# Performance work log

Measured on AMD Instinct MI355X. Metric: run time of the kernel, lower is better.

The kernel has to match this reference:

```python
import jax, jax.numpy as jnp
import numpy as np

B, D, T, K = 16, 512, 4096, 1024

def setup_inputs() -> dict:
    key = jax.random.key(0)
    kx, kc = jax.random.split(key)
    x = jax.random.normal(kx, (B, D, T), dtype=jnp.float32)
    codebook = jax.random.normal(kc, (K, D), dtype=jnp.float32)
    return {"x": x, "codebook": codebook}

def reference(x, codebook):
    # x: [B, D, T] -> xt: [B, T, D]
    xt = jnp.transpose(x, (0, 2, 1))
    x_sq = jnp.sum(xt * xt, axis=-1, keepdims=True)          # [B, T, 1]
    c_sq = jnp.sum(codebook * codebook, axis=-1)             # [K]
    cross = jnp.einsum('btd,kd->btk', xt, codebook)          # [B, T, K]
    dist = x_sq - 2.0 * cross + c_sq                         # [B, T, K]
    indexes = jnp.argmin(dist, axis=2)                       # [B, T] int
    quantized = codebook[indexes]                            # [B, T, D]
    quantized = jnp.transpose(quantized, (0, 2, 1))          # [B, D, T]
    return quantized, indexes
```

## Files before the change

kernel.cpp:

```cpp
#include <hip/hip_runtime.h>

#define BB 16
#define DD 512
#define TT 4096
#define KK 1024

typedef _Float16 h16;
typedef __attribute__((ext_vector_type(8))) _Float16 half8;
typedef __attribute__((ext_vector_type(4))) float float4v;

#define XTH_OFF 0ull
#define XTL_OFF 67108864ull
#define CBH_OFF 134217728ull
#define CBL_OFF 135266304ull
#define CSQ_OFF 136314880ull
#define WS_NEED (136314880ull + 4096ull)

#define GLOAD_LDS16(g, l) __builtin_amdgcn_global_load_lds( \
    (const __attribute__((address_space(1))) void*)(g),      \
    (__attribute__((address_space(3))) void*)(l), 16, 0, 0)

__global__ void csq_kernel(const float* __restrict__ cb, float* __restrict__ csq) {
    int wave = threadIdx.x >> 6;
    int lane = threadIdx.x & 63;
    int row  = blockIdx.x * 4 + wave;
    const float* r = cb + (size_t)row * DD;
    float s = 0.f;
    #pragma unroll
    for (int i = 0; i < DD / 64; ++i) { float v = r[lane + i * 64]; s += v * v; }
    #pragma unroll
    for (int off = 32; off; off >>= 1) s += __shfl_down(s, off, 64);
    if (lane == 0) csq[row] = s;
}

__global__ __launch_bounds__(256) void split_x_kernel(const float* __restrict__ x,
                                                      h16* __restrict__ xth,
                                                      h16* __restrict__ xtl) {
    __shared__ float xs[32][132];
    const int tb = blockIdx.x, dcb = blockIdx.y, b = blockIdx.z;
    const int tid = threadIdx.x;
    const int t0 = tb * 128, d0 = dcb * 32;
    const float* xp = x + ((size_t)b * DD + d0) * TT + t0;
    #pragma unroll
    for (int j = 0; j < 4; ++j) {
        int i4 = tid + 256 * j;
        int dd = i4 >> 5, c4 = (i4 & 31) << 2;
        *(float4*)&xs[dd][c4] = *(const float4*)(xp + (size_t)dd * TT + c4);
    }
    __syncthreads();
    const int r = tid >> 1;
    const int ch = (tid & 1) * 16;
    h16 hv[16], lv[16];
    #pragma unroll
    for (int i = 0; i < 16; ++i) {
        float v = xs[ch + i][r];
        h16 h = (h16)v;
        hv[i] = h;
        lv[i] = (h16)(v - (float)h);
    }
    size_t o = (((size_t)(b * 32 + tb) * 16) + dcb) * 4096 + (size_t)tid * 16;
    *(half8*)(xth + o)     = *(half8*)&hv[0];
    *(half8*)(xth + o + 8) = *(half8*)&hv[8];
    *(half8*)(xtl + o)     = *(half8*)&lv[0];
    *(half8*)(xtl + o + 8) = *(half8*)&lv[8];
}

__global__ __launch_bounds__(256) void split_cb_kernel(const float* __restrict__ cb,
                                                       h16* __restrict__ cbh,
                                                       h16* __restrict__ cbl) {
    const int kb = blockIdx.x >> 4, dcb = blockIdx.x & 15;
    const int tid = threadIdx.x;
    const float* cp = cb + ((size_t)kb * 128) * DD + dcb * 32;
    h16* oh = cbh + ((size_t)(kb * 16 + dcb)) * 4096;
    h16* ol = cbl + ((size_t)(kb * 16 + dcb)) * 4096;
    #pragma unroll
    for (int j = 0; j < 4; ++j) {
        int i4 = tid + 256 * j;
        int rr = i4 >> 3, c4 = (i4 & 7) << 2;
        float4 v = *(const float4*)(cp + (size_t)rr * DD + c4);
        float vv[4] = {v.x, v.y, v.z, v.w};
        h16 h[4], l[4];
        #pragma unroll
        for (int i = 0; i < 4; ++i) {
            h[i] = (h16)vv[i];
            l[i] = (h16)(vv[i] - (float)h[i]);
        }
        *(ushort4*)(oh + rr * 32 + c4) = *(ushort4*)h;
        *(ushort4*)(ol + rr * 32 + c4) = *(ushort4*)l;
    }
}

__global__ __launch_bounds__(512, 4) void mfma_argmin_kernel(
    const h16* __restrict__ xth, const h16* __restrict__ xtl,
    const h16* __restrict__ cbh, const h16* __restrict__ cbl,
    const float* __restrict__ csq, const float* __restrict__ cb,
    float* __restrict__ idx_f_out, float* __restrict__ out) {

    __shared__ h16 ash[2][4096];
    __shared__ h16 asl[2][4096];
    __shared__ h16 bsh[2][4096];
    __shared__ h16 bsl[2][4096];
    __shared__ float redv[4][128];
    __shared__ int   redi[4][128];

    const int tid = threadIdx.x;
    const int wid = tid >> 6, lane = tid & 63;
    const int wm = wid & 1;
    const int wn = wid >> 1;
    const int tb = blockIdx.x, b = blockIdx.y;
    const int t0 = tb * 128;
    const int c  = lane & 15;
    const int q  = lane >> 4;

    const h16* aH = xth + ((size_t)(b * 32 + tb) * 16) * 4096;
    const h16* aL = xtl + ((size_t)(b * 32 + tb) * 16) * 4096;

    const int soff = tid * 8;

    GLOAD_LDS16(aH  + soff,        &ash[0][soff]);
    GLOAD_LDS16(aL  + soff,        &asl[0][soff]);
    GLOAD_LDS16(cbh + soff,        &bsh[0][soff]);
    GLOAD_LDS16(cbl + soff,        &bsl[0][soff]);
    GLOAD_LDS16(aH  + 4096 + soff, &ash[1][soff]);
    GLOAD_LDS16(aL  + 4096 + soff, &asl[1][soff]);
    GLOAD_LDS16(cbh + 4096 + soff, &bsh[1][soff]);
    GLOAD_LDS16(cbl + 4096 + soff, &bsl[1][soff]);

    float best[16];
    int   bidx[16];
    #pragma unroll
    for (int i = 0; i < 16; ++i) { best[i] = 3.4e38f; bidx[i] = 0; }

    for (int kci = 0; kci < 8; ++kci) {
        float4v acc[4][2];
        #pragma unroll
        for (int m = 0; m < 4; ++m)
            #pragma unroll
            for (int n = 0; n < 2; ++n)
                acc[m][n] = (float4v){0.f, 0.f, 0.f, 0.f};

        for (int dcb = 0; dcb < 16; ++dcb) {
            const int g  = kci * 16 + dcb;
            const int bf = g & 1;

            if (g < 127) asm volatile("s_waitcnt vmcnt(4)" ::: "memory");
            else         asm volatile("s_waitcnt vmcnt(0)" ::: "memory");
            __builtin_amdgcn_s_barrier();

            const int doff = q * 8;
            half8 Ah[4], Al[4], Bh[2], Bl[2];
            #pragma unroll
            for (int m = 0; m < 4; ++m) {
                int row = wm * 64 + m * 16 + c;
                Ah[m] = *(const half8*)(&ash[bf][row * 32 + doff]);
                Al[m] = *(const half8*)(&asl[bf][row * 32 + doff]);
            }
            #pragma unroll
            for (int n = 0; n < 2; ++n) {
                int row = wn * 32 + n * 16 + c;
                Bh[n] = *(const half8*)(&bsh[bf][row * 32 + doff]);
                Bl[n] = *(const half8*)(&bsl[bf][row * 32 + doff]);
            }

            asm volatile("s_waitcnt lgkmcnt(0)" ::: "memory");
            __builtin_amdgcn_s_barrier();

            if (g + 2 < 128) {
                const int gn = g + 2;
                const int kn = gn >> 4, dn = gn & 15;
                GLOAD_LDS16(aH + (size_t)dn * 4096 + soff,                    &ash[bf][soff]);
                GLOAD_LDS16(aL + (size_t)dn * 4096 + soff,                    &asl[bf][soff]);
                GLOAD_LDS16(cbh + ((size_t)(kn * 16 + dn)) * 4096 + soff,     &bsh[bf][soff]);
                GLOAD_LDS16(cbl + ((size_t)(kn * 16 + dn)) * 4096 + soff,     &bsl[bf][soff]);
            }

            #pragma unroll
            for (int n = 0; n < 2; ++n)
                #pragma unroll
                for (int m = 0; m < 4; ++m)
                    acc[m][n] = __builtin_amdgcn_mfma_f32_16x16x32_f16(Ah[m], Bh[n], acc[m][n], 0, 0, 0);
            #pragma unroll
            for (int n = 0; n < 2; ++n)
                #pragma unroll
                for (int m = 0; m < 4; ++m)
                    acc[m][n] = __builtin_amdgcn_mfma_f32_16x16x32_f16(Ah[m], Bl[n], acc[m][n], 0, 0, 0);
            #pragma unroll
            for (int n = 0; n < 2; ++n)
                #pragma unroll
                for (int m = 0; m < 4; ++m)
                    acc[m][n] = __builtin_amdgcn_mfma_f32_16x16x32_f16(Al[m], Bh[n], acc[m][n], 0, 0, 0);
        }

        #pragma unroll
        for (int n = 0; n < 2; ++n) {
            int kg = kci * 128 + wn * 32 + n * 16 + c;
            float cq = csq[kg];
            #pragma unroll
            for (int m = 0; m < 4; ++m)
                #pragma unroll
                for (int r = 0; r < 4; ++r) {
                    float s = fmaf(-2.0f, acc[m][n][r], cq);
                    int slot = m * 4 + r;
                    if (s < best[slot]) { best[slot] = s; bidx[slot] = kg; }
                }
        }
    }

    #pragma unroll
    for (int slot = 0; slot < 16; ++slot) {
        float v = best[slot]; int i = bidx[slot];
        #pragma unroll
        for (int d = 1; d < 16; d <<= 1) {
            float pv = __shfl_xor(v, d);
            int   pi = __shfl_xor(i, d);
            if (pv < v || (pv == v && pi < i)) { v = pv; i = pi; }
        }
        if (c == 0) {
            int m = slot >> 2, r = slot & 3;
            int tl = wm * 64 + m * 16 + q * 4 + r;
            redv[wn][tl] = v; redi[wn][tl] = i;
        }
    }
    __syncthreads();
    if (tid < 128) {
        float v0 = redv[0][tid]; int i0 = redi[0][tid];
        #pragma unroll
        for (int gi = 1; gi < 4; ++gi) {
            float v1 = redv[gi][tid]; int i1 = redi[gi][tid];
            if (v1 < v0 || (v1 == v0 && i1 < i0)) { v0 = v1; i0 = i1; }
        }
        idx_f_out[(size_t)b * TT + t0 + tid] = (float)i0;
        redi[0][tid] = i0;
    }
    __syncthreads();

    const int tl = tid & 127, dg = tid >> 7;
    const int k = redi[0][tl];
    const float* row = cb + (size_t)k * DD + dg * 128;
    float* ob = out + ((size_t)b * DD + dg * 128) * TT + t0 + tl;
    #pragma unroll 4
    for (int i = 0; i < 32; ++i) {
        float4 v = *(const float4*)(row + i * 4);
        ob[(size_t)(i * 4 + 0) * TT] = v.x;
        ob[(size_t)(i * 4 + 1) * TT] = v.y;
        ob[(size_t)(i * 4 + 2) * TT] = v.z;
        ob[(size_t)(i * 4 + 3) * TT] = v.w;
    }
}

__global__ void gather_kernel(const float* __restrict__ cb,
                              const float* __restrict__ idx_f,
                              float* __restrict__ out) {
    int b  = blockIdx.y;
    int t  = blockIdx.x * 256 + threadIdx.x;
    int d0 = blockIdx.z * (DD / 4);
    int k  = (int)idx_f[(size_t)b * TT + t];
    const float* row = cb + (size_t)k * DD;
    float* ob = out + (size_t)b * DD * TT + t;
    #pragma unroll 8
    for (int d = d0; d < d0 + DD / 4; ++d)
        ob[(size_t)d * TT] = row[d];
}

__global__ __launch_bounds__(256) void argmin_fp32_kernel(
    const float* __restrict__ x, const float* __restrict__ cb,
    const float* __restrict__ csq, float* __restrict__ idx_f_out) {

    __shared__ float xs[32][128];
    __shared__ float cs[32][132];

    const int tid = threadIdx.x;
    const int b = blockIdx.y;
    const int t_blk = blockIdx.x * 128;
    const int tq = tid & 15, kq = tid >> 4;
    const int t0 = tq * 8, k0 = kq * 8;
    const float* xb = x + (size_t)b * DD * TT;

    float best[8]; int bidx[8];
    #pragma unroll
    for (int i = 0; i < 8; ++i) { best[i] = 3.4e38f; bidx[i] = 0; }

    for (int kc = 0; kc < KK; kc += 128) {
        float acc[8][8];
        #pragma unroll
        for (int i = 0; i < 8; ++i)
            #pragma unroll
            for (int j = 0; j < 8; ++j) acc[i][j] = 0.f;
        for (int dc = 0; dc < DD; dc += 32) {
            __syncthreads();
            #pragma unroll
            for (int j = 0; j < 4; ++j) {
                int i4 = tid + 256 * j;
                int dd = i4 >> 5, tp = (i4 & 31) << 2;
                *(float4*)&xs[dd][tp] =
                    *(const float4*)(xb + (size_t)(dc + dd) * TT + t_blk + tp);
            }
            #pragma unroll
            for (int j = 0; j < 4; ++j) {
                int i4 = tid + 256 * j;
                int kk = i4 >> 3, dq = (i4 & 7) << 2;
                float4 v = *(const float4*)(cb + (size_t)(kc + kk) * DD + dc + dq);
                cs[dq + 0][kk] = v.x; cs[dq + 1][kk] = v.y;
                cs[dq + 2][kk] = v.z; cs[dq + 3][kk] = v.w;
            }
            __syncthreads();
            #pragma unroll 8
            for (int dd = 0; dd < 32; ++dd) {
                float a[8], bv[8];
                *(float4*)&a[0]  = *(const float4*)&xs[dd][t0];
                *(float4*)&a[4]  = *(const float4*)&xs[dd][t0 + 4];
                *(float4*)&bv[0] = *(const float4*)&cs[dd][k0];
                *(float4*)&bv[4] = *(const float4*)&cs[dd][k0 + 4];
                #pragma unroll
                for (int i = 0; i < 8; ++i)
                    #pragma unroll
                    for (int j = 0; j < 8; ++j)
                        acc[i][j] = fmaf(a[i], bv[j], acc[i][j]);
            }
        }
        #pragma unroll
        for (int j = 0; j < 8; ++j) {
            int kg = kc + k0 + j;
            float cq = csq[kg];
            #pragma unroll
            for (int i = 0; i < 8; ++i) {
                float s = cq - 2.0f * acc[i][j];
                if (s < best[i]) { best[i] = s; bidx[i] = kg; }
            }
        }
    }
    __syncthreads();
    float* rbest = &xs[0][0];
    int*   ridx  = (int*)&cs[0][0];
    #pragma unroll
    for (int i = 0; i < 8; ++i) {
        rbest[kq * 128 + t0 + i] = best[i];
        ridx [kq * 128 + t0 + i] = bidx[i];
    }
    __syncthreads();
    if (tid < 128) {
        float bv = rbest[tid]; int bi = ridx[tid];
        #pragma unroll
        for (int g = 1; g < 16; ++g) {
            float v = rbest[g * 128 + tid]; int ii = ridx[g * 128 + tid];
            if (v < bv || (v == bv && ii < bi)) { bv = v; bi = ii; }
        }
        idx_f_out[(size_t)b * TT + t_blk + tid] = (float)bi;
    }
}

extern "C" void kernel_launch(void* const* d_in, const int* in_sizes, int n_in,
                              void* d_out, int out_size, void* d_ws, size_t ws_size,
                              hipStream_t stream) {
    const float* x  = (const float*)d_in[0];
    const float* cb = (const float*)d_in[1];
    float* out   = (float*)d_out;
    float* idx_f = out + (size_t)BB * DD * TT;

    if (ws_size >= WS_NEED) {
        h16* xth = (h16*)((char*)d_ws + XTH_OFF);
        h16* xtl = (h16*)((char*)d_ws + XTL_OFF);
        h16* cbh = (h16*)((char*)d_ws + CBH_OFF);
        h16* cbl = (h16*)((char*)d_ws + CBL_OFF);
        float* csq = (float*)((char*)d_ws + CSQ_OFF);

        csq_kernel<<<KK / 4, 256, 0, stream>>>(cb, csq);
        split_cb_kernel<<<128, 256, 0, stream>>>(cb, cbh, cbl);
        split_x_kernel<<<dim3(TT / 128, DD / 32, BB), 256, 0, stream>>>(x, xth, xtl);
        mfma_argmin_kernel<<<dim3(TT / 128, BB), 512, 0, stream>>>(
            xth, xtl, cbh, cbl, csq, cb, idx_f, out);
    } else {
        float* csq = (float*)d_ws;
        csq_kernel<<<KK / 4, 256, 0, stream>>>(cb, csq);
        argmin_fp32_kernel<<<dim3(TT / 128, BB), 256, 0, stream>>>(x, cb, csq, idx_f);
        gather_kernel<<<dim3(TT / 256, BB, 4), 256, 0, stream>>>(cb, idx_f, out);
    }
}
```

Measured before the change: 488.8 us.

## Software-pipeline A-fragment LDS reads across MFMA phases with double-buffered registers

Restructures the main loop into a manually unrolled two-stage body. The A fragments for the next step are prefetched into a second register set between the two MFMA halves, and the B reads, barriers and global-to-LDS loads are interleaved with the MFMA groups. It also adds s_setprio around the MFMA bursts and sched_barriers to pin the instruction order. The intent is to hide LDS read latency and barrier stalls behind matrix work, at the cost of higher register pressure and an extra barrier per step.

```diff
diff --git a/kernel.cpp b/kernel.cpp
--- a/kernel.cpp
+++ b/kernel.cpp
@@ -116,6 +116,13 @@
     const h16* aL = xtl + ((size_t)(b * 32 + tb) * 16) * 4096;
 
     const int soff = tid * 8;
+    const int doff = q * 8;
+
+    int arow[4], brow[2];
+    #pragma unroll
+    for (int m = 0; m < 4; ++m) arow[m] = (wm * 64 + m * 16 + c) * 32 + doff;
+    #pragma unroll
+    for (int n = 0; n < 2; ++n) brow[n] = (wn * 32 + n * 16 + c) * 32 + doff;
 
     GLOAD_LDS16(aH  + soff,        &ash[0][soff]);
     GLOAD_LDS16(aL  + soff,        &asl[0][soff]);
@@ -131,80 +138,99 @@
     #pragma unroll
     for (int i = 0; i < 16; ++i) { best[i] = 3.4e38f; bidx[i] = 0; }
 
-    for (int kci = 0; kci < 8; ++kci) {
-        float4v acc[4][2];
-        #pragma unroll
-        for (int m = 0; m < 4; ++m)
-            #pragma unroll
-            for (int n = 0; n < 2; ++n)
-                acc[m][n] = (float4v){0.f, 0.f, 0.f, 0.f};
-
-        for (int dcb = 0; dcb < 16; ++dcb) {
-            const int g  = kci * 16 + dcb;
-            const int bf = g & 1;
-
-            if (g < 127) asm volatile("s_waitcnt vmcnt(4)" ::: "memory");
-            else         asm volatile("s_waitcnt vmcnt(0)" ::: "memory");
-            __builtin_amdgcn_s_barrier();
-
-            const int doff = q * 8;
-            half8 Ah[4], Al[4], Bh[2], Bl[2];
-            #pragma unroll
-            for (int m = 0; m < 4; ++m) {
-                int row = wm * 64 + m * 16 + c;
-                Ah[m] = *(const half8*)(&ash[bf][row * 32 + doff]);
-                Al[m] = *(const half8*)(&asl[bf][row * 32 + doff]);
-            }
+    float4v acc[4][2];
+    #pragma unroll
+    for (int m = 0; m < 4; ++m)
+        #pragma unroll
+        for (int n = 0; n < 2; ++n)
+            acc[m][n] = (float4v){0.f, 0.f, 0.f, 0.f};
+
+    asm volatile("s_waitcnt vmcnt(4)" ::: "memory");
+    __builtin_amdgcn_s_barrier();
+
+    half8 Ah0[4], Al0[4], Ah1[4], Al1[4];
+    #pragma unroll
+    for (int m = 0; m < 4; ++m) {
+        Ah0[m] = *(const half8*)(&ash[0][arow[m]]);
+        Al0[m] = *(const half8*)(&asl[0][arow[m]]);
+    }
+
+#define MFMA16(a, bv, d) d = __builtin_amdgcn_mfma_f32_16x16x32_f16(a, bv, d, 0, 0, 0)
+
+#define BODY(G, BF, AhC, AlC, AhN, AlN) do {                                     \
+                                    \
+    half8 Bh0 = *(const half8*)(&bsh[BF][brow[0]]);                              \
+    half8 Bl0 = *(const half8*)(&bsl[BF][brow[0]]);                              \
+    half8 Bh1 = *(const half8*)(&bsh[BF][brow[1]]);                              \
+    half8 Bl1 = *(const half8*)(&bsl[BF][brow[1]]);                              \
+    asm volatile("s_waitcnt lgkmcnt(0)" ::: "memory");                           \
+    __builtin_amdgcn_s_barrier();       \
+    __builtin_amdgcn_sched_barrier(0);                                           \
+    if ((G) + 2 < 128) {                  \
+        const int dn_ = ((G) + 2) & 15;                                          \
+        GLOAD_LDS16(aH + (size_t)dn_ * 4096 + soff,        &ash[BF][soff]);      \
+        GLOAD_LDS16(aL + (size_t)dn_ * 4096 + soff,        &asl[BF][soff]);      \
+        GLOAD_LDS16(cbh + (size_t)((G) + 2) * 4096 + soff, &bsh[BF][soff]);      \
+        GLOAD_LDS16(cbl + (size_t)((G) + 2) * 4096 + soff, &bsl[BF][soff]);      \
+    }                                                                            \
+    __builtin_amdgcn_s_setprio(1);               \
+    MFMA16(AhC[0], Bh0, acc[0][0]); MFMA16(AhC[1], Bh0, acc[1][0]);              \
+    MFMA16(AhC[2], Bh0, acc[2][0]); MFMA16(AhC[3], Bh0, acc[3][0]);              \
+    MFMA16(AhC[0], Bh1, acc[0][1]); MFMA16(AhC[1], Bh1, acc[1][1]);              \
+    MFMA16(AhC[2], Bh1, acc[2][1]); MFMA16(AhC[3], Bh1, acc[3][1]);              \
+    MFMA16(AhC[0], Bl0, acc[0][0]); MFMA16(AhC[1], Bl0, acc[1][0]);              \
+    MFMA16(AhC[2], Bl0, acc[2][0]); MFMA16(AhC[3], Bl0, acc[3][0]);              \
+    __builtin_amdgcn_s_setprio(0);                                               \
+    if ((G) + 2 < 128)      asm volatile("s_waitcnt vmcnt(4)" ::: "memory");     \
+    else if ((G) + 1 < 128) asm volatile("s_waitcnt vmcnt(0)" ::: "memory");     \
+    __builtin_amdgcn_s_barrier();           \
+    __builtin_amdgcn_sched_barrier(0);                                           \
+    if ((G) + 1 < 128) {                     \
+        _Pragma("unroll")                                                        \
+        for (int m = 0; m < 4; ++m) {                                            \
+            AhN[m] = *(const half8*)(&ash[(BF) ^ 1][arow[m]]);                   \
+            AlN[m] = *(const half8*)(&asl[(BF) ^ 1][arow[m]]);                   \
+        }                                                                        \
+    }                                                                            \
+    __builtin_amdgcn_s_setprio(1);               \
+    MFMA16(AhC[0], Bl1, acc[0][1]); MFMA16(AhC[1], Bl1, acc[1][1]);              \
+    MFMA16(AhC[2], Bl1, acc[2][1]); MFMA16(AhC[3], Bl1, acc[3][1]);              \
+    MFMA16(AlC[0], Bh0, acc[0][0]); MFMA16(AlC[1], Bh0, acc[1][0]);              \
+    MFMA16(AlC[2], Bh0, acc[2][0]); MFMA16(AlC[3], Bh0, acc[3][0]);              \
+    MFMA16(AlC[0], Bh1, acc[0][1]); MFMA16(AlC[1], Bh1, acc[1][1]);              \
+    MFMA16(AlC[2], Bh1, acc[2][1]); MFMA16(AlC[3], Bh1, acc[3][1]);              \
+    __builtin_amdgcn_s_setprio(0);                                               \
+} while (0)
+
+    for (int gp = 0; gp < 64; ++gp) {
+        const int g0 = gp * 2;
+        BODY(g0,     0, Ah0, Al0, Ah1, Al1);
+        BODY(g0 + 1, 1, Ah1, Al1, Ah0, Al0);
+
+        if ((gp & 7) == 7) {
+            const int kci = gp >> 3;
             #pragma unroll
             for (int n = 0; n < 2; ++n) {
-                int row = wn * 32 + n * 16 + c;
-                Bh[n] = *(const half8*)(&bsh[bf][row * 32 + doff]);
-                Bl[n] = *(const half8*)(&bsl[bf][row * 32 + doff]);
-            }
-
-            asm volatile("s_waitcnt lgkmcnt(0)" ::: "memory");
-            __builtin_amdgcn_s_barrier();
-
-            if (g + 2 < 128) {
-                const int gn = g + 2;
-                const int kn = gn >> 4, dn = gn & 15;
-                GLOAD_LDS16(aH + (size_t)dn * 4096 + soff,                    &ash[bf][soff]);
-                GLOAD_LDS16(aL + (size_t)dn * 4096 + soff,                    &asl[bf][soff]);
-                GLOAD_LDS16(cbh + ((size_t)(kn * 16 + dn)) * 4096 + soff,     &bsh[bf][soff]);
-                GLOAD_LDS16(cbl + ((size_t)(kn * 16 + dn)) * 4096 + soff,     &bsl[bf][soff]);
-            }
-
-            #pragma unroll
-            for (int n = 0; n < 2; ++n)
+                int kg = kci * 128 + wn * 32 + n * 16 + c;
+                float cq = csq[kg];
                 #pragma unroll
                 for (int m = 0; m < 4; ++m)
-                    acc[m][n] = __builtin_amdgcn_mfma_f32_16x16x32_f16(Ah[m], Bh[n], acc[m][n], 0, 0, 0);
-            #pragma unroll
-            for (int n = 0; n < 2; ++n)
-                #pragma unroll
-                for (int m = 0; m < 4; ++m)
-                    acc[m][n] = __builtin_amdgcn_mfma_f32_16x16x32_f16(Ah[m], Bl[n], acc[m][n], 0, 0, 0);
-            #pragma unroll
-            for (int n = 0; n < 2; ++n)
-                #pragma unroll
-                for (int m = 0; m < 4; ++m)
-                    acc[m][n] = __builtin_amdgcn_mfma_f32_16x16x32_f16(Al[m], Bh[n], acc[m][n], 0, 0, 0);
-        }
-
-        #pragma unroll
-        for (int n = 0; n < 2; ++n) {
-            int kg = kci * 128 + wn * 32 + n * 16 + c;
-            float cq = csq[kg];
+                    #pragma unroll
+                    for (int r = 0; r < 4; ++r) {
+                        float s = fmaf(-2.0f, acc[m][n][r], cq);
+                        int slot = m * 4 + r;
+                        if (s < best[slot]) { best[slot] = s; bidx[slot] = kg; }
+                    }
+            }
             #pragma unroll
             for (int m = 0; m < 4; ++m)
                 #pragma unroll
-                for (int r = 0; r < 4; ++r) {
-                    float s = fmaf(-2.0f, acc[m][n][r], cq);
-                    int slot = m * 4 + r;
-                    if (s < best[slot]) { best[slot] = s; bidx[slot] = kg; }
-                }
-        }
-    }
+                for (int n = 0; n < 2; ++n)
+                    acc[m][n] = (float4v){0.f, 0.f, 0.f, 0.f};
+        }
+    }
+#undef BODY
+#undef MFMA16
 
     #pragma unroll
     for (int slot = 0; slot < 16; ++slot) {
```

Measured after the change: 580.4 us. +18.7%, slower.

## Widen codebook tile per block from 128 to 256 codes to halve A reloads

Applied to the files above, without the earlier changes.

Each block now processes 256 codebook entries per K-chunk instead of 128, with each wave computing a 64x64 tile (4x4 MFMA accumulators) instead of 64x32. This halves the number of times the x tile is staged through LDS and raises MFMA work per LDS load. In exchange, B-side LDS buffers double, accumulator registers double, and launch bounds drop from 4 to 2 blocks per CU, lowering occupancy.

```diff
diff --git a/kernel.cpp b/kernel.cpp
--- a/kernel.cpp
+++ b/kernel.cpp
@@ -90,7 +90,7 @@
     }
 }
 
-__global__ __launch_bounds__(512, 4) void mfma_argmin_kernel(
+__global__ __launch_bounds__(512, 2) void mfma_argmin_kernel(
     const h16* __restrict__ xth, const h16* __restrict__ xtl,
     const h16* __restrict__ cbh, const h16* __restrict__ cbl,
     const float* __restrict__ csq, const float* __restrict__ cb,
@@ -98,8 +98,8 @@
 
     __shared__ h16 ash[2][4096];
     __shared__ h16 asl[2][4096];
-    __shared__ h16 bsh[2][4096];
-    __shared__ h16 bsl[2][4096];
+    __shared__ h16 bsh[2][8192];
+    __shared__ h16 bsl[2][8192];
     __shared__ float redv[4][128];
     __shared__ int   redi[4][128];
 
@@ -117,94 +117,100 @@
 
     const int soff = tid * 8;
 
-    GLOAD_LDS16(aH  + soff,        &ash[0][soff]);
-    GLOAD_LDS16(aL  + soff,        &asl[0][soff]);
-    GLOAD_LDS16(cbh + soff,        &bsh[0][soff]);
-    GLOAD_LDS16(cbl + soff,        &bsl[0][soff]);
-    GLOAD_LDS16(aH  + 4096 + soff, &ash[1][soff]);
-    GLOAD_LDS16(aL  + 4096 + soff, &asl[1][soff]);
-    GLOAD_LDS16(cbh + 4096 + soff, &bsh[1][soff]);
-    GLOAD_LDS16(cbl + 4096 + soff, &bsl[1][soff]);
+#define STAGE(GI, BF) do {                                                   \
+        const int dn_ = (GI) & 15, kc_ = (GI) >> 4;                          \
+        const size_t b0_ = ((size_t)(kc_ * 32 + dn_)) * 4096;                \
+        const size_t b1_ = ((size_t)(kc_ * 32 + 16 + dn_)) * 4096;          \
+        GLOAD_LDS16(aH + (size_t)dn_ * 4096 + soff, &ash[BF][soff]);         \
+        GLOAD_LDS16(aL + (size_t)dn_ * 4096 + soff, &asl[BF][soff]);         \
+        GLOAD_LDS16(cbh + b0_ + soff, &bsh[BF][soff]);                       \
+        GLOAD_LDS16(cbh + b1_ + soff, &bsh[BF][4096 + soff]);                \
+        GLOAD_LDS16(cbl + b0_ + soff, &bsl[BF][soff]);                       \
+        GLOAD_LDS16(cbl + b1_ + soff, &bsl[BF][4096 + soff]);                \
+    } while (0)
+
+    STAGE(0, 0);
+    STAGE(1, 1);
 
     float best[16];
     int   bidx[16];
     #pragma unroll
     for (int i = 0; i < 16; ++i) { best[i] = 3.4e38f; bidx[i] = 0; }
 
-    for (int kci = 0; kci < 8; ++kci) {
-        float4v acc[4][2];
-        #pragma unroll
-        for (int m = 0; m < 4; ++m)
-            #pragma unroll
-            for (int n = 0; n < 2; ++n)
-                acc[m][n] = (float4v){0.f, 0.f, 0.f, 0.f};
-
-        for (int dcb = 0; dcb < 16; ++dcb) {
-            const int g  = kci * 16 + dcb;
-            const int bf = g & 1;
-
-            if (g < 127) asm volatile("s_waitcnt vmcnt(4)" ::: "memory");
-            else         asm volatile("s_waitcnt vmcnt(0)" ::: "memory");
-            __builtin_amdgcn_s_barrier();
-
-            const int doff = q * 8;
-            half8 Ah[4], Al[4], Bh[2], Bl[2];
-            #pragma unroll
-            for (int m = 0; m < 4; ++m) {
-                int row = wm * 64 + m * 16 + c;
-                Ah[m] = *(const half8*)(&ash[bf][row * 32 + doff]);
-                Al[m] = *(const half8*)(&asl[bf][row * 32 + doff]);
-            }
-            #pragma unroll
-            for (int n = 0; n < 2; ++n) {
-                int row = wn * 32 + n * 16 + c;
-                Bh[n] = *(const half8*)(&bsh[bf][row * 32 + doff]);
-                Bl[n] = *(const half8*)(&bsl[bf][row * 32 + doff]);
-            }
-
-            asm volatile("s_waitcnt lgkmcnt(0)" ::: "memory");
-            __builtin_amdgcn_s_barrier();
-
-            if (g + 2 < 128) {
-                const int gn = g + 2;
-                const int kn = gn >> 4, dn = gn & 15;
-                GLOAD_LDS16(aH + (size_t)dn * 4096 + soff,                    &ash[bf][soff]);
-                GLOAD_LDS16(aL + (size_t)dn * 4096 + soff,                    &asl[bf][soff]);
-                GLOAD_LDS16(cbh + ((size_t)(kn * 16 + dn)) * 4096 + soff,     &bsh[bf][soff]);
-                GLOAD_LDS16(cbl + ((size_t)(kn * 16 + dn)) * 4096 + soff,     &bsl[bf][soff]);
-            }
-
-            #pragma unroll
-            for (int n = 0; n < 2; ++n)
+    float4v acc[4][4];
+    #pragma unroll
+    for (int m = 0; m < 4; ++m)
+        #pragma unroll
+        for (int n = 0; n < 4; ++n)
+            acc[m][n] = (float4v){0.f, 0.f, 0.f, 0.f};
+
+    const int doff = q * 8;
+
+    for (int gi = 0; gi < 64; ++gi) {
+        const int bf = gi & 1;
+
+        if (gi < 63) asm volatile("s_waitcnt vmcnt(6)" ::: "memory");
+        else         asm volatile("s_waitcnt vmcnt(0)" ::: "memory");
+        __builtin_amdgcn_s_barrier();
+
+        half8 Ah[4], Al[4], Bh[4], Bl[4];
+        #pragma unroll
+        for (int m = 0; m < 4; ++m) {
+            int row = wm * 64 + m * 16 + c;
+            Ah[m] = *(const half8*)(&ash[bf][row * 32 + doff]);
+            Al[m] = *(const half8*)(&asl[bf][row * 32 + doff]);
+        }
+        #pragma unroll
+        for (int n = 0; n < 4; ++n) {
+            int row = wn * 64 + n * 16 + c;
+            Bh[n] = *(const half8*)(&bsh[bf][row * 32 + doff]);
+            Bl[n] = *(const half8*)(&bsl[bf][row * 32 + doff]);
+        }
+
+        asm volatile("s_waitcnt lgkmcnt(0)" ::: "memory");
+        __builtin_amdgcn_s_barrier();
+
+        if (gi + 2 < 64) STAGE(gi + 2, bf);
+
+        #pragma unroll
+        for (int n = 0; n < 4; ++n)
+            #pragma unroll
+            for (int m = 0; m < 4; ++m)
+                acc[m][n] = __builtin_amdgcn_mfma_f32_16x16x32_f16(Ah[m], Bh[n], acc[m][n], 0, 0, 0);
+        #pragma unroll
+        for (int n = 0; n < 4; ++n)
+            #pragma unroll
+            for (int m = 0; m < 4; ++m)
+                acc[m][n] = __builtin_amdgcn_mfma_f32_16x16x32_f16(Ah[m], Bl[n], acc[m][n], 0, 0, 0);
+        #pragma unroll
+        for (int n = 0; n < 4; ++n)
+            #pragma unroll
+            for (int m = 0; m < 4; ++m)
+                acc[m][n] = __builtin_amdgcn_mfma_f32_16x16x32_f16(Al[m], Bh[n], acc[m][n], 0, 0, 0);
+
+        if ((gi & 15) == 15) {
+            const int kci = gi >> 4;
+            #pragma unroll
+            for (int n = 0; n < 4; ++n) {
+                int kg = kci * 256 + wn * 64 + n * 16 + c;
+                float cq = csq[kg];
                 #pragma unroll
                 for (int m = 0; m < 4; ++m)
-                    acc[m][n] = __builtin_amdgcn_mfma_f32_16x16x32_f16(Ah[m], Bh[n], acc[m][n], 0, 0, 0);
-            #pragma unroll
-            for (int n = 0; n < 2; ++n)
-                #pragma unroll
-                for (int m = 0; m < 4; ++m)
-                    acc[m][n] = __builtin_amdgcn_mfma_f32_16x16x32_f16(Ah[m], Bl[n], acc[m][n], 0, 0, 0);
-            #pragma unroll
-            for (int n = 0; n < 2; ++n)
-                #pragma unroll
-                for (int m = 0; m < 4; ++m)
-                    acc[m][n] = __builtin_amdgcn_mfma_f32_16x16x32_f16(Al[m], Bh[n], acc[m][n], 0, 0, 0);
-        }
-
-        #pragma unroll
-        for (int n = 0; n < 2; ++n) {
-            int kg = kci * 128 + wn * 32 + n * 16 + c;
-            float cq = csq[kg];
+                    #pragma unroll
+                    for (int r = 0; r < 4; ++r) {
+                        float s = fmaf(-2.0f, acc[m][n][r], cq);
+                        int slot = m * 4 + r;
+                        if (s < best[slot]) { best[slot] = s; bidx[slot] = kg; }
+                    }
+            }
             #pragma unroll
             for (int m = 0; m < 4; ++m)
                 #pragma unroll
-                for (int r = 0; r < 4; ++r) {
-                    float s = fmaf(-2.0f, acc[m][n][r], cq);
-                    int slot = m * 4 + r;
-                    if (s < best[slot]) { best[slot] = s; bidx[slot] = kg; }
-                }
-        }
-    }
+                for (int n = 0; n < 4; ++n)
+                    acc[m][n] = (float4v){0.f, 0.f, 0.f, 0.f};
+        }
+    }
+#undef STAGE
 
     #pragma unroll
     for (int slot = 0; slot < 16; ++slot) {
```

New measurement: 484.2 us. No clear change (-0.9%).
